# Kernel optimization log

Measured on AMD Instinct MI355X. Metric: run time of the kernel, lower is better.

Reference implementation:

```python
import jax, jax.numpy as jnp
import numpy as np

D_MODEL = 1024
N_HEADS = 16
D_HEAD = D_MODEL // N_HEADS
FF = 4 * D_MODEL
B, S = 1, 2048
ROPE_BASE = 10000.0
LN_EPS = 1e-5


def setup_inputs() -> dict:
    key = jax.random.key(0)
    ks = jax.random.split(key, 12)
    sd = 0.02
    return {
        "x": jax.random.normal(ks[0], (B, S, D_MODEL), dtype=jnp.float32),
        # weights stored [in, out]
        "w_qkv": jax.random.normal(ks[1], (D_MODEL, 3 * D_MODEL), dtype=jnp.float32) * sd,
        "w_attn": jax.random.normal(ks[2], (D_MODEL, D_MODEL), dtype=jnp.float32) * sd,
        "b_attn": jnp.zeros((D_MODEL,), dtype=jnp.float32),
        "w_ff1": jax.random.normal(ks[3], (D_MODEL, FF), dtype=jnp.float32) * sd,
        "b_ff1": jnp.zeros((FF,), dtype=jnp.float32),
        "w_ff2": jax.random.normal(ks[4], (FF, D_MODEL), dtype=jnp.float32) * sd,
        "b_ff2": jnp.zeros((D_MODEL,), dtype=jnp.float32),
        "ln1_g": jnp.ones((D_MODEL,), dtype=jnp.float32),
        "ln1_b": jnp.zeros((D_MODEL,), dtype=jnp.float32),
        "ln2_g": jnp.ones((D_MODEL,), dtype=jnp.float32),
        "ln2_b": jnp.zeros((D_MODEL,), dtype=jnp.float32),
    }


def _layernorm(x, g, b):
    mu = jnp.mean(x, axis=-1, keepdims=True)
    var = jnp.mean(jnp.square(x - mu), axis=-1, keepdims=True)
    return (x - mu) * jax.lax.rsqrt(var + LN_EPS) * g + b


def _rope_cos_sin(seq_len, d_head, dtype):
    # scale=1.0 -> dynamic YaRN degenerates to vanilla RoPE with mscale=1
    inv_freq = 1.0 / (ROPE_BASE ** (jnp.arange(0, d_head, 2, dtype=jnp.float32) / d_head))
    pos = jnp.arange(seq_len, dtype=jnp.float32)
    freqs = pos[:, None] * inv_freq[None, :]          # [S, D/2]
    emb = jnp.concatenate([freqs, freqs], axis=-1)    # [S, D]
    return jnp.cos(emb).astype(dtype), jnp.sin(emb).astype(dtype)


def _rotate_half(x):
    x1, x2 = jnp.split(x, 2, axis=-1)
    return jnp.concatenate([-x2, x1], axis=-1)


def _apply_rope(q, k, cos, sin):
    # q,k: [B,S,H,D]; cos/sin: [S,D]
    c = cos[None, :, None, :]
    s = sin[None, :, None, :]
    return q * c + _rotate_half(q) * s, k * c + _rotate_half(k) * s


def _block(x, w_qkv, w_attn, b_attn, w_ff1, b_ff1, w_ff2, b_ff2,
           ln1_g, ln1_b, ln2_g, ln2_b):
    b, s, d = x.shape
    # --- attention sub-block (pre-norm) ---
    h = _layernorm(x, ln1_g, ln1_b)
    qkv = h @ w_qkv                                   # [B,S,3D]
    xq, xk, xv = jnp.split(qkv, 3, axis=-1)
    xq = xq.reshape(b, s, N_HEADS, D_HEAD)
    xk = xk.reshape(b, s, N_HEADS, D_HEAD)
    xv = xv.reshape(b, s, N_HEADS, D_HEAD)
    cos, sin = _rope_cos_sin(s, D_HEAD, x.dtype)
    xq, xk = _apply_rope(xq, xk, cos, sin)
    scale = 1.0 / np.sqrt(D_HEAD)
    scores = jnp.einsum("bqhd,bkhd->bhqk", xq, xk) * scale
    causal = jnp.tril(jnp.ones((s, s), dtype=bool))
    scores = jnp.where(causal[None, None], scores, jnp.finfo(scores.dtype).min)
    probs = jax.nn.softmax(scores, axis=-1)
    att = jnp.einsum("bhqk,bkhd->bqhd", probs, xv).reshape(b, s, d)
    x = x + (att @ w_attn + b_attn)
    # --- feed-forward sub-block (pre-norm) ---
    h2 = _layernorm(x, ln2_g, ln2_b)
    ff = jax.nn.gelu(h2 @ w_ff1 + b_ff1, approximate=False) @ w_ff2 + b_ff2
    return x + ff


def reference(x, w_qkv, w_attn, b_attn, w_ff1, b_ff1, w_ff2, b_ff2,
              ln1_g, ln1_b, ln2_g, ln2_b):
    return _block(x, w_qkv, w_attn, b_attn, w_ff1, b_ff1, w_ff2, b_ff2,
                  ln1_g, ln1_b, ln2_g, ln2_b)
```

## Files before the change

kernel.cpp:

```cpp
#include <hip/hip_runtime.h>
#include <hip/hip_bf16.h>
#include <stdint.h>

#define DM   1024
#define SEQ  2048
#define NH   16
#define DH   64
#define FFD  4096

typedef float  f32x4  __attribute__((ext_vector_type(4)));
typedef float  f32x16 __attribute__((ext_vector_type(16)));
typedef __bf16 bf16x8 __attribute__((ext_vector_type(8)));
typedef unsigned short u16;
typedef unsigned short u16x4v __attribute__((ext_vector_type(4)));
typedef unsigned short u16x8 __attribute__((ext_vector_type(8)));

__device__ __forceinline__ u16 f2bf(float f){
    unsigned int u = __builtin_bit_cast(unsigned int, f);
    u = u + 0x7FFFu + ((u >> 16) & 1u);
    return (u16)(u >> 16);
}
__device__ __forceinline__ float bf2f(u16 v){
    unsigned int u = ((unsigned int)v) << 16;
    return __builtin_bit_cast(float, u);
}
__device__ __forceinline__ f32x4 zero4(){ f32x4 v; v[0]=0.f;v[1]=0.f;v[2]=0.f;v[3]=0.f; return v; }
__device__ __forceinline__ unsigned int cvtpk(float lo, float hi){
    unsigned int r;
    asm("v_cvt_pk_bf16_f32 %0, %1, %2" : "=v"(r) : "v"(lo), "v"(hi));
    return r;
}

__device__ __forceinline__ void gload_lds16(const void* g, void* l){
    __builtin_amdgcn_global_load_lds(
        (const __attribute__((address_space(1))) unsigned int*)(uintptr_t)g,
        (__attribute__((address_space(3))) unsigned int*)(uintptr_t)l,
        16, 0, 0);
}

__global__ __launch_bounds__(256) void transall_k(const float* __restrict__ s0, u16* __restrict__ d0,
                                                  const float* __restrict__ s1, u16* __restrict__ d1,
                                                  const float* __restrict__ s2, u16* __restrict__ d2,
                                                  const float* __restrict__ s3, u16* __restrict__ d3){
    __shared__ float tile[64][65];
    const int b = blockIdx.x;
    const float* src; u16* dst; int K, N, bx, by;
    if (b < 768)      { src = s0; dst = d0; K = 1024; N = 3072; bx = b % 48;          by = b / 48; }
    else if (b < 1024){ src = s1; dst = d1; K = 1024; N = 1024; bx = (b-768) % 16;    by = (b-768) / 16; }
    else if (b < 2048){ src = s2; dst = d2; K = 1024; N = 4096; bx = (b-1024) % 64;   by = (b-1024) / 64; }
    else              { src = s3; dst = d3; K = 4096; N = 1024; bx = (b-2048) % 16;   by = (b-2048) / 16; }
    const int n0 = bx * 64, k0 = by * 64;
    const int t = threadIdx.x;
#pragma unroll
    for (int i = 0; i < 16; ++i){
        int idx = t + i * 256;
        int r = idx >> 6, c = idx & 63;
        tile[r][c] = src[(size_t)(k0 + r) * N + n0 + c];
    }
    __syncthreads();
#pragma unroll
    for (int i = 0; i < 16; ++i){
        int idx = t + i * 256;
        int r = idx >> 6, c = idx & 63;
        dst[(size_t)(n0 + r) * K + k0 + c] = f2bf(tile[c][r]);
    }
}

__global__ __launch_bounds__(256) void ln_k(const float* __restrict__ in,
                                            const float* __restrict__ gw,
                                            const float* __restrict__ bw,
                                            u16* __restrict__ out){
    const int row = blockIdx.x, t = threadIdx.x;
    f32x4 vv = *((const f32x4*)(in + (size_t)row * DM) + t);
    float v[4];
#pragma unroll
    for (int j = 0; j < 4; ++j) v[j] = vv[j];
    float s = 0.f, ss = 0.f;
#pragma unroll
    for (int j = 0; j < 4; ++j){ s += v[j]; ss += v[j] * v[j]; }
#pragma unroll
    for (int off = 1; off < 64; off <<= 1){
        s  += __shfl_xor(s,  off, 64);
        ss += __shfl_xor(ss, off, 64);
    }
    __shared__ float rs_[4], rss_[4];
    const int w = t >> 6;
    if ((t & 63) == 0){ rs_[w] = s; rss_[w] = ss; }
    __syncthreads();
    s  = rs_[0] + rs_[1] + rs_[2] + rs_[3];
    ss = rss_[0] + rss_[1] + rss_[2] + rss_[3];
    const float mean = s * (1.f / DM);
    const float var  = ss * (1.f / DM) - mean * mean;
    const float rstd = rsqrtf(var + 1e-5f);
#pragma unroll
    for (int j = 0; j < 4; ++j){
        int c = t * 4 + j;
        out[(size_t)row * DM + c] = f2bf((v[j] - mean) * rstd * gw[c] + bw[c]);
    }
}

template<int TM, int TN, int WR, int WC, int EPI>
__global__ __launch_bounds__(256) void gemm_k(const u16* __restrict__ A,
                                              const u16* __restrict__ Bt,
                                              const float* __restrict__ bias,
                                              const float* __restrict__ resid,
                                              void* __restrict__ out,
                                              u16* __restrict__ qout,
                                              u16* __restrict__ kout,
                                              u16* __restrict__ vout,
                                              int M, int N, int K){
    constexpr int MR   = TM / WR / 16;
    constexpr int NR   = TN / WC / 16;
    constexpr int AISS = (TM * 64) / 4096;
    constexpr int BISS = (TN * 64) / 4096;
    __shared__ u16 ldsAll[2 * TM * 32 + 2 * TN * 32];
    u16* ldsA = ldsAll;
    u16* ldsB = ldsAll + 2 * TM * 32;
    const int t = threadIdx.x;
    const int L = t & 63, w = t >> 6;
    const int g = L >> 4, li = L & 15;
    const int wr = w / WC, wc = w % WC;
    const int rowbase = wr * (TM / WR);
    const int colbase = wc * (TN / WC);
    const int nxb  = M / TM;
    const int nper = (int)gridDim.x >> 3;
    const int jswz = ((int)blockIdx.x & 7) * nper + ((int)blockIdx.x >> 3);
    const int brow = (jswz % nxb) * TM, bcol = (jswz / nxb) * TN;

    const u16* aPtr = A  + (size_t)brow * K;
    const u16* bPtr = Bt + (size_t)bcol * K;

    f32x4 acc[MR][NR];
#pragma unroll
    for (int m = 0; m < MR; ++m)
#pragma unroll
        for (int n = 0; n < NR; ++n) acc[m][n] = zero4();

    auto STAGE = [&](int buf, int ko){
#pragma unroll
        for (int i = 0; i < AISS; ++i){
            int o = i * 256 + t;
            gload_lds16(aPtr + (size_t)(o >> 2) * K + (o & 3) * 8 + ko, &ldsA[buf * TM * 32 + o * 8]);
        }
#pragma unroll
        for (int i = 0; i < BISS; ++i){
            int o = i * 256 + t;
            gload_lds16(bPtr + (size_t)(o >> 2) * K + (o & 3) * 8 + ko, &ldsB[buf * TN * 32 + o * 8]);
        }
    };

    const int KT = K >> 5;
    int cur = 0;
    STAGE(0, 0);
    __syncthreads();
    for (int kt = 0; kt < KT; ++kt){
        if (kt + 1 < KT) STAGE(cur ^ 1, (kt + 1) * 32);
        bf16x8 af[MR], bfr[NR];
#pragma unroll
        for (int m = 0; m < MR; ++m)
            af[m]  = *(const bf16x8*)&ldsA[cur * TM * 32 + (rowbase + m * 16 + li) * 32 + g * 8];
#pragma unroll
        for (int n = 0; n < NR; ++n)
            bfr[n] = *(const bf16x8*)&ldsB[cur * TN * 32 + (colbase + n * 16 + li) * 32 + g * 8];
#pragma unroll
        for (int m = 0; m < MR; ++m)
#pragma unroll
            for (int n = 0; n < NR; ++n)
                acc[m][n] = __builtin_amdgcn_mfma_f32_16x16x32_bf16(af[m], bfr[n], acc[m][n], 0, 0, 0);
        __syncthreads();
        cur ^= 1;
    }

    if constexpr (EPI == 4){
        const int colabs = bcol + colbase;
        const int part = colabs >> 10;
        if (part < 2){
            u16* dst = (part == 0) ? qout : kout;
            const int h = (colabs >> 6) & 15;
            float freq[2];
#pragma unroll
            for (int n = 0; n < 2; ++n)
                freq[n] = powf(10000.f, -(float)(n * 16 + li) * (1.f / 32.f));
#pragma unroll
            for (int m = 0; m < MR; ++m)
#pragma unroll
                for (int r = 0; r < 4; ++r){
                    const int srow = brow + rowbase + m * 16 + g * 4 + r;
                    const size_t rb = ((size_t)h * SEQ + srow) * 64;
#pragma unroll
                    for (int n = 0; n < 2; ++n){
                        const int i = n * 16 + li;
                        float lo = acc[m][n][r], hi = acc[m][n + 2][r];
                        float sn, cs;
                        sincosf((float)srow * freq[n], &sn, &cs);
                        dst[rb + i]      = f2bf(lo * cs - hi * sn);
                        dst[rb + i + 32] = f2bf(hi * cs + lo * sn);
                    }
                }
        } else {
            u16* tileT = ldsAll;
            __syncthreads();
#pragma unroll
            for (int m = 0; m < MR; ++m)
#pragma unroll
                for (int n = 0; n < NR; ++n)
#pragma unroll
                    for (int r = 0; r < 4; ++r){
                        const int row = rowbase + m * 16 + g * 4 + r;
                        const int col = colbase + n * 16 + li;
                        tileT[col * 72 + row] = f2bf(acc[m][n][r]);
                    }
            __syncthreads();
            const int dv = t >> 1, half = t & 1;
            const int habs = ((bcol + dv) >> 6) & 15;
            const int dvl = dv & 63;
            u16* vrow = vout + ((size_t)habs * 64 + dvl) * SEQ + brow + half * 32;
#pragma unroll
            for (int j = 0; j < 4; ++j)
                *(u16x8*)(vrow + j * 8) = *(const u16x8*)&tileT[dv * 72 + half * 32 + j * 8];
        }
        return;
    }

#pragma unroll
    for (int m = 0; m < MR; ++m)
#pragma unroll
        for (int n = 0; n < NR; ++n)
#pragma unroll
            for (int r = 0; r < 4; ++r){
                const int row = brow + rowbase + m * 16 + g * 4 + r;
                const int col = bcol + colbase + n * 16 + li;
                float v = acc[m][n][r];
                if constexpr (EPI == 1){
                    v += bias[col] + resid[(size_t)row * N + col];
                    ((float*)out)[(size_t)row * N + col] = v;
                } else if constexpr (EPI == 2){
                    v += bias[col];
                    v = 0.5f * v * (1.f + erff(v * 0.70710678f));
                    ((u16*)out)[(size_t)row * N + col] = f2bf(v);
                } else {
                    v += bias[col] + resid[(size_t)row * N + col];
                    ((float*)out)[(size_t)row * N + col] = v;
                }
            }
}

#define CHT 8
__global__ __launch_bounds__(256) void attn_k(const u16* __restrict__ Qh,
                                              const u16* __restrict__ Kh,
                                              const u16* __restrict__ VT,
                                              u16* __restrict__ Opart,
                                              float* __restrict__ ml){
    const int t = threadIdx.x, w = t >> 6, L = t & 63;
    const int bid = blockIdx.x;
    const int xcd = bid & 7;
    const int lj  = (bid >> 3) * 4 + w;
    const int h   = xcd * 2 + (lj & 1);
    const int jd  = lj >> 1;
    int g = 7, rem = jd;
    while (rem >= 8 * (g + 1)){ rem -= 8 * (g + 1); --g; }
    const int gp1 = g + 1;
    const int qt = 8 * g + 7 - rem / gp1;
    const int c  = rem % gp1;
    const int t0 = c * CHT;
    const int tEnd = min(t0 + CHT, qt + 1);
    const int l31 = L & 31, H = L >> 5;
    const int qbase = qt * 32;

    const u16* kB = Kh + (size_t)h * SEQ * 64;
    const u16* vB = VT + (size_t)h * 64 * SEQ;

    const u16* qrow = Qh + ((size_t)h * SEQ + qbase + l31) * 64 + H * 8;
    bf16x8 qf0 = *(const bf16x8*)(qrow);
    bf16x8 qf1 = *(const bf16x8*)(qrow + 16);
    bf16x8 qf2 = *(const bf16x8*)(qrow + 32);
    bf16x8 qf3 = *(const bf16x8*)(qrow + 48);

    const u16* krow0 = kB + (size_t)(t0 * 32 + l31) * 64 + H * 8;
    bf16x8 kc0 = *(const bf16x8*)(krow0);
    bf16x8 kc1 = *(const bf16x8*)(krow0 + 16);
    bf16x8 kc2 = *(const bf16x8*)(krow0 + 32);
    bf16x8 kc3 = *(const bf16x8*)(krow0 + 48);

    f32x16 O0, O1;
#pragma unroll
    for (int i = 0; i < 16; ++i){ O0[i] = 0.f; O1[i] = 0.f; }
    float m = -3.0e4f, lsum = 0.f;

    for (int tt = t0; tt < tEnd; ++tt){
        const u16* va0 = vB + (size_t)l31 * SEQ + tt * 32 + H * 8;
        const u16* va1 = va0 + (size_t)32 * SEQ;
        bf16x8 v00 = *(const bf16x8*)(va0);
        bf16x8 v01 = *(const bf16x8*)(va0 + 16);
        bf16x8 v10 = *(const bf16x8*)(va1);
        bf16x8 v11 = *(const bf16x8*)(va1 + 16);

        f32x16 st;
#pragma unroll
        for (int i = 0; i < 16; ++i) st[i] = 0.f;
        st = __builtin_amdgcn_mfma_f32_32x32x16_bf16(kc0, qf0, st, 0, 0, 0);
        st = __builtin_amdgcn_mfma_f32_32x32x16_bf16(kc1, qf1, st, 0, 0, 0);
        st = __builtin_amdgcn_mfma_f32_32x32x16_bf16(kc2, qf2, st, 0, 0, 0);
        st = __builtin_amdgcn_mfma_f32_32x32x16_bf16(kc3, qf3, st, 0, 0, 0);

        const bool more = (tt + 1 < tEnd);
        bf16x8 kn0, kn1, kn2, kn3;
        if (more){
            const u16* krow = kB + (size_t)((tt + 1) * 32 + l31) * 64 + H * 8;
            kn0 = *(const bf16x8*)(krow);
            kn1 = *(const bf16x8*)(krow + 16);
            kn2 = *(const bf16x8*)(krow + 32);
            kn3 = *(const bf16x8*)(krow + 48);
        }

        const bool diag = (tt == qt);
        float sv[16];
#pragma unroll
        for (int i = 0; i < 16; ++i){
            float x = st[i] * 0.125f;
            if (diag){
                int kkl = (i & 3) + 8 * (i >> 2) + 4 * H;
                if (kkl > l31) x = -3.0e4f;
            }
            sv[i] = x;
        }
        float smax = sv[0];
#pragma unroll
        for (int i = 1; i < 16; ++i) smax = fmaxf(smax, sv[i]);
        smax = fmaxf(smax, __shfl_xor(smax, 32, 64));
        const float nm = fmaxf(m, smax);
        const float alpha = __expf(m - nm);
        m = nm;
        float ps = 0.f;
#pragma unroll
        for (int i = 0; i < 16; ++i){ sv[i] = __expf(sv[i] - m); ps += sv[i]; }
        ps += __shfl_xor(ps, 32, 64);
        lsum = lsum * alpha + ps;
#pragma unroll
        for (int i = 0; i < 16; ++i){ O0[i] *= alpha; O1[i] *= alpha; }

        unsigned int A0 = cvtpk(sv[0],  sv[1]),  A1 = cvtpk(sv[2],  sv[3]);
        unsigned int B0 = cvtpk(sv[4],  sv[5]),  B1 = cvtpk(sv[6],  sv[7]);
        unsigned int C0 = cvtpk(sv[8],  sv[9]),  C1 = cvtpk(sv[10], sv[11]);
        unsigned int D0 = cvtpk(sv[12], sv[13]), D1 = cvtpk(sv[14], sv[15]);
        unsigned int eA0 = (unsigned int)__shfl_xor((int)A0, 32, 64);
        unsigned int eA1 = (unsigned int)__shfl_xor((int)A1, 32, 64);
        unsigned int eB0 = (unsigned int)__shfl_xor((int)B0, 32, 64);
        unsigned int eB1 = (unsigned int)__shfl_xor((int)B1, 32, 64);
        unsigned int eC0 = (unsigned int)__shfl_xor((int)C0, 32, 64);
        unsigned int eC1 = (unsigned int)__shfl_xor((int)C1, 32, 64);
        unsigned int eD0 = (unsigned int)__shfl_xor((int)D0, 32, 64);
        unsigned int eD1 = (unsigned int)__shfl_xor((int)D1, 32, 64);
        union Uw { unsigned int w[4]; bf16x8 v; };
        Uw f0, f1;
        f0.w[0] = H ? eB0 : A0;  f0.w[1] = H ? eB1 : A1;
        f0.w[2] = H ? B0  : eA0; f0.w[3] = H ? B1  : eA1;
        f1.w[0] = H ? eD0 : C0;  f1.w[1] = H ? eD1 : C1;
        f1.w[2] = H ? D0  : eC0; f1.w[3] = H ? D1  : eC1;

        O0 = __builtin_amdgcn_mfma_f32_32x32x16_bf16(v00, f0.v, O0, 0, 0, 0);
        O0 = __builtin_amdgcn_mfma_f32_32x32x16_bf16(v01, f1.v, O0, 0, 0, 0);
        O1 = __builtin_amdgcn_mfma_f32_32x32x16_bf16(v10, f0.v, O1, 0, 0, 0);
        O1 = __builtin_amdgcn_mfma_f32_32x32x16_bf16(v11, f1.v, O1, 0, 0, 0);

        if (more){ kc0 = kn0; kc1 = kn1; kc2 = kn2; kc3 = kn3; }
    }

    const int jobd = h * 288 + jd;
    const size_t ob = (size_t)jobd * (32 * 64);
    const int q = l31;
#pragma unroll
    for (int f = 0; f < 2; ++f){
        const int dv0 = f * 32;
#pragma unroll
        for (int k = 0; k < 4; ++k){
            u16x4v pkv;
#pragma unroll
            for (int e = 0; e < 4; ++e)
                pkv[e] = f2bf(f == 0 ? O0[k * 4 + e] : O1[k * 4 + e]);
            *(u16x4v*)(Opart + ob + (size_t)q * 64 + dv0 + 8 * k + 4 * H) = pkv;
        }
    }
    if (H == 0){
        ml[((size_t)jobd * 32 + q) * 2]     = m;
        ml[((size_t)jobd * 32 + q) * 2 + 1] = lsum;
    }
}

__global__ __launch_bounds__(256) void combine_k(const u16* __restrict__ Opart,
                                                 const float* __restrict__ ml,
                                                 u16* __restrict__ att){
    const int qt = blockIdx.x, h = blockIdx.y;
    const int g = qt >> 3, gp1 = g + 1;
    const int off = 8 * (36 - ((gp1 * (g + 2)) >> 1));
    const int jd0 = off + (8 * g + 7 - qt) * gp1;
    const int j0 = h * 288 + jd0;
    const int nact = gp1;
    const int t = threadIdx.x;
    const int q = t >> 3, dv0 = (t & 7) * 8;

    float m = -3.0e30f;
    for (int cc = 0; cc < nact; ++cc)
        m = fmaxf(m, ml[((size_t)(j0 + cc) * 32 + q) * 2]);
    float Ls = 0.f;
    float o[8];
#pragma unroll
    for (int j = 0; j < 8; ++j) o[j] = 0.f;
    for (int cc = 0; cc < nact; ++cc){
        const float mv = ml[((size_t)(j0 + cc) * 32 + q) * 2];
        const float lv = ml[((size_t)(j0 + cc) * 32 + q) * 2 + 1];
        const float wgt = __expf(mv - m);
        Ls += wgt * lv;
        const u16* src = Opart + ((size_t)(j0 + cc) * 32 + q) * 64 + dv0;
        u16x8 a = *(const u16x8*)src;
#pragma unroll
        for (int e = 0; e < 8; ++e) o[e] += wgt * bf2f(a[e]);
    }
    const float inv = 1.f / Ls;
    const int qg = qt * 32 + q;
#pragma unroll
    for (int j = 0; j < 8; ++j)
        att[(size_t)qg * DM + h * 64 + dv0 + j] = f2bf(o[j] * inv);
}

extern "C" void kernel_launch(void* const* d_in, const int* in_sizes, int n_in,
                              void* d_out, int out_size, void* d_ws, size_t ws_size,
                              hipStream_t stream){
    (void)in_sizes; (void)n_in; (void)out_size; (void)ws_size;
    const float* x      = (const float*)d_in[0];
    const float* w_qkv  = (const float*)d_in[1];
    const float* w_attn = (const float*)d_in[2];
    const float* b_attn = (const float*)d_in[3];
    const float* w_ff1  = (const float*)d_in[4];
    const float* b_ff1  = (const float*)d_in[5];
    const float* w_ff2  = (const float*)d_in[6];
    const float* b_ff2  = (const float*)d_in[7];
    const float* ln1g   = (const float*)d_in[8];
    const float* ln1b   = (const float*)d_in[9];
    const float* ln2g   = (const float*)d_in[10];
    const float* ln2b   = (const float*)d_in[11];

    char* ws = (char*)d_ws;
    const size_t MB = 1u << 20;
    u16*   T1    = (u16*)(ws + 0);
    u16*   T2    = (u16*)(ws + 6  * MB);
    u16*   T3    = (u16*)(ws + 8  * MB);
    u16*   T4    = (u16*)(ws + 16 * MB);
    u16*   h1    = (u16*)(ws + 24 * MB);
    u16*   Qh    = (u16*)(ws + 28 * MB);
    u16*   Kh    = (u16*)(ws + 32 * MB);
    u16*   VT    = (u16*)(ws + 36 * MB);
    u16*   Opart = (u16*)(ws + 40 * MB);
    float* mlbuf = (float*)(ws + 59 * MB);
    u16*   att   = (u16*)(ws + 0);
    float* x2    = (float*)(ws + 40 * MB);
    u16*   h2    = (u16*)(ws + 4  * MB);
    u16*   ff    = (u16*)(ws + 24 * MB);

    transall_k<<<3072, 256, 0, stream>>>(w_qkv, T1, w_attn, T2, w_ff1, T3, w_ff2, T4);
    ln_k<<<SEQ, 256, 0, stream>>>(x, ln1g, ln1b, h1);
    gemm_k<64,128,2,2,4><<<768, 256, 0, stream>>>(h1, T1, nullptr, nullptr, nullptr,
                                                  Qh, Kh, VT, SEQ, 3072, 1024);
    attn_k<<<1152, 256, 0, stream>>>(Qh, Kh, VT, Opart, mlbuf);
    combine_k<<<dim3(64, 16), 256, 0, stream>>>(Opart, mlbuf, att);
    gemm_k<64,64,2,2,1><<<512, 256, 0, stream>>>(att, T2, b_attn, x, x2,
                                                 nullptr, nullptr, nullptr, SEQ, 1024, 1024);
    ln_k<<<SEQ, 256, 0, stream>>>(x2, ln2g, ln2b, h2);
    gemm_k<64,128,1,4,2><<<1024, 256, 0, stream>>>(h2, T3, b_ff1, nullptr, ff,
                                                   nullptr, nullptr, nullptr, SEQ, 4096, 1024);
    gemm_k<64,64,2,2,3><<<512, 256, 0, stream>>>(ff, T4, b_ff2, x2, (float*)d_out,
                                                 nullptr, nullptr, nullptr, SEQ, 1024, 4096);
}
```

Measured before the change: 195.6 us.

## Store Q/K/V in MFMA-fragment-tiled layout for coalesced attention loads

The QKV GEMM epilogue now writes Q, K and V^T into a tiled layout where each 32-row tile is laid out so every lane's 8-element fragment sits contiguously and consecutive lanes read adjacent 16-byte chunks. The attention kernel's Q/K/V loads then become fully coalesced 512/1024-element strided blocks instead of row-strided gathers. This is meant to cut memory transaction count in the attention inner loop. The tradeoff is scattered 2-byte stores in the RoPE epilogue and a producer/consumer layout coupling.

New measurement: 178.4 us, median of 2. -8.8%, faster.

```diff
diff --git a/kernel.cpp b/kernel.cpp
--- a/kernel.cpp
+++ b/kernel.cpp
@@ -186,15 +186,15 @@
 #pragma unroll
                 for (int r = 0; r < 4; ++r){
                     const int srow = brow + rowbase + m * 16 + g * 4 + r;
-                    const size_t rb = ((size_t)h * SEQ + srow) * 64;
+                    const size_t tb = (size_t)(h * 64 + (srow >> 5)) * 2048
+                                    + (li >> 3) * 256 + (srow & 31) * 8 + (li & 7);
 #pragma unroll
                     for (int n = 0; n < 2; ++n){
-                        const int i = n * 16 + li;
                         float lo = acc[m][n][r], hi = acc[m][n + 2][r];
                         float sn, cs;
                         sincosf((float)srow * freq[n], &sn, &cs);
-                        dst[rb + i]      = f2bf(lo * cs - hi * sn);
-                        dst[rb + i + 32] = f2bf(hi * cs + lo * sn);
+                        dst[tb + n * 512]       = f2bf(lo * cs - hi * sn);
+                        dst[tb + (n + 2) * 512] = f2bf(hi * cs + lo * sn);
                     }
                 }
         } else {
@@ -214,10 +214,13 @@
             const int dv = t >> 1, half = t & 1;
             const int habs = ((bcol + dv) >> 6) & 15;
             const int dvl = dv & 63;
-            u16* vrow = vout + ((size_t)habs * 64 + dvl) * SEQ + brow + half * 32;
+            const int f = dvl >> 5, dv5 = dvl & 31;
+            const int tt = (brow >> 5) + half;
+            u16* vbase = vout + (size_t)(habs * 64 + tt) * 2048 + f * 256 + dv5 * 8;
 #pragma unroll
             for (int j = 0; j < 4; ++j)
-                *(u16x8*)(vrow + j * 8) = *(const u16x8*)&tileT[dv * 72 + half * 32 + j * 8];
+                *(u16x8*)(vbase + (j >> 1) * 1024 + (j & 1) * 512)
+                    = *(const u16x8*)&tileT[dv * 72 + half * 32 + j * 8];
         }
         return;
     }
@@ -265,22 +268,22 @@
     const int t0 = c * CHT;
     const int tEnd = min(t0 + CHT, qt + 1);
     const int l31 = L & 31, H = L >> 5;
-    const int qbase = qt * 32;
-
-    const u16* kB = Kh + (size_t)h * SEQ * 64;
-    const u16* vB = VT + (size_t)h * 64 * SEQ;
-
-    const u16* qrow = Qh + ((size_t)h * SEQ + qbase + l31) * 64 + H * 8;
-    bf16x8 qf0 = *(const bf16x8*)(qrow);
-    bf16x8 qf1 = *(const bf16x8*)(qrow + 16);
-    bf16x8 qf2 = *(const bf16x8*)(qrow + 32);
-    bf16x8 qf3 = *(const bf16x8*)(qrow + 48);
-
-    const u16* krow0 = kB + (size_t)(t0 * 32 + l31) * 64 + H * 8;
-    bf16x8 kc0 = *(const bf16x8*)(krow0);
-    bf16x8 kc1 = *(const bf16x8*)(krow0 + 16);
-    bf16x8 kc2 = *(const bf16x8*)(krow0 + 32);
-    bf16x8 kc3 = *(const bf16x8*)(krow0 + 48);
+
+    const size_t hT = (size_t)h * 64;
+    const int lane_off = H * 256 + l31 * 8;
+    const int vlane_off = H * 512 + l31 * 8;
+
+    const u16* qB = Qh + (hT + qt) * 2048 + lane_off;
+    bf16x8 qf0 = *(const bf16x8*)(qB);
+    bf16x8 qf1 = *(const bf16x8*)(qB + 512);
+    bf16x8 qf2 = *(const bf16x8*)(qB + 1024);
+    bf16x8 qf3 = *(const bf16x8*)(qB + 1536);
+
+    const u16* kB0 = Kh + (hT + t0) * 2048 + lane_off;
+    bf16x8 kc0 = *(const bf16x8*)(kB0);
+    bf16x8 kc1 = *(const bf16x8*)(kB0 + 512);
+    bf16x8 kc2 = *(const bf16x8*)(kB0 + 1024);
+    bf16x8 kc3 = *(const bf16x8*)(kB0 + 1536);
 
     f32x16 O0, O1;
 #pragma unroll
@@ -288,12 +291,11 @@
     float m = -3.0e4f, lsum = 0.f;
 
     for (int tt = t0; tt < tEnd; ++tt){
-        const u16* va0 = vB + (size_t)l31 * SEQ + tt * 32 + H * 8;
-        const u16* va1 = va0 + (size_t)32 * SEQ;
-        bf16x8 v00 = *(const bf16x8*)(va0);
-        bf16x8 v01 = *(const bf16x8*)(va0 + 16);
-        bf16x8 v10 = *(const bf16x8*)(va1);
-        bf16x8 v11 = *(const bf16x8*)(va1 + 16);
+        const u16* vB = VT + (hT + tt) * 2048 + vlane_off;
+        bf16x8 v00 = *(const bf16x8*)(vB);
+        bf16x8 v01 = *(const bf16x8*)(vB + 1024);
+        bf16x8 v10 = *(const bf16x8*)(vB + 256);
+        bf16x8 v11 = *(const bf16x8*)(vB + 1280);
 
         f32x16 st;
 #pragma unroll
@@ -306,11 +308,11 @@
         const bool more = (tt + 1 < tEnd);
         bf16x8 kn0, kn1, kn2, kn3;
         if (more){
-            const u16* krow = kB + (size_t)((tt + 1) * 32 + l31) * 64 + H * 8;
-            kn0 = *(const bf16x8*)(krow);
-            kn1 = *(const bf16x8*)(krow + 16);
-            kn2 = *(const bf16x8*)(krow + 32);
-            kn3 = *(const bf16x8*)(krow + 48);
+            const u16* kBn = Kh + (hT + tt + 1) * 2048 + lane_off;
+            kn0 = *(const bf16x8*)(kBn);
+            kn1 = *(const bf16x8*)(kBn + 512);
+            kn2 = *(const bf16x8*)(kBn + 1024);
+            kn3 = *(const bf16x8*)(kBn + 1536);
         }
 
         const bool diag = (tt == qt);
```
